# Performance work log

Measured on AMD Instinct MI355X. Metric: run time of the kernel, lower is better.

## Reference

```python
import jax, jax.numpy as jnp
import numpy as np

N_HEAD = 12


def build_mask(T, N):
    """Boolean mask, True = blocked. Mirrors st_mask construction for
    text_mask_mode='none', domain_present=None, text_to_motion_attn=False."""
    L = 3 * T + 5 * N
    r = jnp.arange(T)
    causal = r[:, None] >= r[None, :]          # allowed (lower-tri incl diag)
    strict = r[:, None] > r[None, :]           # allowed (strictly lower)
    m = jnp.zeros((L, L), dtype=bool)
    ml = 3 * T
    # motion-motion region starts fully blocked, then 7 sub-blocks opened
    m = m.at[:ml, :ml].set(True)
    m = m.at[0:T, 0:T].set(~causal)
    m = m.at[T:2 * T, 0:T].set(~causal)
    m = m.at[T:2 * T, T:2 * T].set(~strict)
    m = m.at[T:2 * T, 2 * T:3 * T].set(~strict)
    m = m.at[2 * T:3 * T, 0:T].set(~causal)
    m = m.at[2 * T:3 * T, T:2 * T].set(~causal)
    m = m.at[2 * T:3 * T, 2 * T:3 * T].set(~strict)
    # motion queries -> text keys: blocked by default
    m = m.at[:ml, ml:].set(True)
    # text queries -> motion keys: blocked (text_to_motion_attn=False)
    m = m.at[ml:, :ml].set(True)
    # text_mask_mode='none': up/down motion rows attend ALL text domains
    m = m.at[T:3 * T, ml:].set(False)
    return m


def setup_inputs() -> dict:
    key = jax.random.key(0)
    ks = jax.random.split(key, 9)
    C = 768
    B, T, N = 4, 512, 16
    L = 3 * T + 5 * N
    s = 1.0 / np.sqrt(C)
    return {
        "x": jax.random.normal(ks[0], (B, L, C), dtype=jnp.float32),
        "Wq": jax.random.normal(ks[1], (C, C), dtype=jnp.float32) * s,
        "bq": jax.random.normal(ks[2], (C,), dtype=jnp.float32) * 0.02,
        "Wk": jax.random.normal(ks[3], (C, C), dtype=jnp.float32) * s,
        "bk": jax.random.normal(ks[4], (C,), dtype=jnp.float32) * 0.02,
        "Wv": jax.random.normal(ks[5], (C, C), dtype=jnp.float32) * s,
        "bv": jax.random.normal(ks[6], (C,), dtype=jnp.float32) * 0.02,
        "Wp": jax.random.normal(ks[7], (C, C), dtype=jnp.float32) * s,
        "bp": jax.random.normal(ks[8], (C,), dtype=jnp.float32) * 0.02,
        "T_motion": 512,
        "N": 16,
    }


def reference(x, Wq, bq, Wk, bk, Wv, bv, Wp, bp, T_motion, N):
    B, L, C = x.shape
    nh = N_HEAD
    hd = C // nh
    # projections (torch Linear: x @ W.T + b)
    q = (x @ Wq.T + bq).reshape(B, L, nh, hd).transpose(0, 2, 1, 3)
    k = (x @ Wk.T + bk).reshape(B, L, nh, hd).transpose(0, 2, 1, 3)
    v = (x @ Wv.T + bv).reshape(B, L, nh, hd).transpose(0, 2, 1, 3)
    att = jnp.einsum('bhqd,bhkd->bhqk', q, k) * (1.0 / np.sqrt(hd))
    mask = build_mask(T_motion, N)                 # [L, L], True = blocked
    att = jnp.where(mask[None, None], -jnp.inf, att)
    att = jax.nn.softmax(att, axis=-1)
    y = jnp.einsum('bhqk,bhkd->bhqd', att, v)      # [B, nh, L, hd]
    y = y.transpose(0, 2, 1, 3).reshape(B, L, C)
    return y @ Wp.T + bp
```

## Files before the change

### kernel.cpp

```cpp
#include <hip/hip_runtime.h>

typedef _Float16 half8_t __attribute__((ext_vector_type(8)));
typedef _Float16 half4_t __attribute__((ext_vector_type(4)));
typedef int      int2_t  __attribute__((ext_vector_type(2)));
typedef float    f32x4   __attribute__((ext_vector_type(4)));

#define L_TOT 1616
#define L_PAD 1664
#define ML    1536
#define TT    512
#define CDIM  768
#define HD    64
#define NH    12
#define MTOT  6464

#define QK_SCALE 0.1803368801f
#define FIXED_M 10.0f

#if __has_builtin(__builtin_amdgcn_exp2f)
#define EXP2F(x) __builtin_amdgcn_exp2f(x)
#else
#define EXP2F(x) __expf((x) * 0.69314718056f)
#endif

typedef __attribute__((address_space(3))) void  as3_void;
typedef const __attribute__((address_space(1))) void as1_void;
__device__ __forceinline__ void gload_lds16(const void* g, void* l) {
  __builtin_amdgcn_global_load_lds((as1_void*)g, (as3_void*)l, 16, 0, 0);
}

__device__ __forceinline__ bool is_blocked(int i, int j) {
  if (j >= L_TOT) return true;
  if (i >= ML) return j < ML;
  if (j >= ML) return i < TT;
  int bi = i >> 9, bj = j >> 9;
  int a = i & 511, c = j & 511;
  if (bi == 0) return !(bj == 0 && c <= a);
  if (bi == 1) {
    if (bj == 0) return !(c <= a);
    return !(c < a);
  }
  if (bj == 2) return !(c < a);
  return !(c <= a);
}

__device__ __forceinline__ void mask_interval(int qrow, int k0, int& lo, int& hi) {
  lo = 0; hi = L_TOT - 1;
  if (qrow >= L_TOT)      { hi = -1; }
  else if (qrow >= ML)    { lo = ML; }
  else if (k0 >= ML)      { }
  else {
    int bi = qrow >> 9, bj = k0 >> 9, a = qrow & 511;
    if (bi == 0 && bj > 0) hi = -1;
    else {
      int strict = (bj > 0 && !(bi == 2 && bj == 1)) ? 1 : 0;
      hi = bj * 512 + a - strict;
    }
  }
}

__global__ __launch_bounds__(256) void cvt_kernel(
    const float* __restrict__ x, const float* __restrict__ wq,
    const float* __restrict__ wk, const float* __restrict__ wv,
    const float* __restrict__ wp, _Float16* __restrict__ Xh,
    _Float16* __restrict__ Wh)
{
  const int XN = MTOT * CDIM, WN = CDIM * CDIM;
  int i = (blockIdx.x * 256 + threadIdx.x) * 4;
  const float* src; _Float16* dst;
  if (i < XN) { src = x + i; dst = Xh + i; }
  else {
    int off = i - XN;
    int which = off / WN, rem = off - which * WN;
    const float* w = (which == 0) ? wq : (which == 1) ? wk : (which == 2) ? wv : wp;
    src = w + rem; dst = Wh + off;
  }
  float4 f = *(const float4*)src;
  half4_t h;
  h[0] = (_Float16)f.x; h[1] = (_Float16)f.y;
  h[2] = (_Float16)f.z; h[3] = (_Float16)f.w;
  *(half4_t*)dst = h;
}

__global__ __launch_bounds__(256) void gemm128_kernel(
    const _Float16* __restrict__ A, const _Float16* __restrict__ W,
    const float* __restrict__ bq, const float* __restrict__ bk,
    const float* __restrict__ bv, const float* __restrict__ bp,
    _Float16* __restrict__ Qh, _Float16* __restrict__ Kh,
    _Float16* __restrict__ Vt, float* __restrict__ Out, int fused)
{
  __shared__ __align__(16) _Float16 As[128 * 64];
  __shared__ __align__(16) _Float16 Bs[128 * 64];
  int tm = blockIdx.x, tn = blockIdx.y;
  int tid = threadIdx.x;
  int w = tid >> 6, lane = tid & 63;
  int wm = w & 1, wn = w >> 1;
  int lr = lane & 15, quad = lane >> 4;
  f32x4 acc[4][4];
#pragma unroll
  for (int i = 0; i < 4; i++)
#pragma unroll
    for (int j = 0; j < 4; j++) acc[i][j] = (f32x4){0.f, 0.f, 0.f, 0.f};
  int glog = ((lane & 7) ^ (lane >> 3)) * 8;
  const _Float16* gA[4]; const _Float16* gB[4];
#pragma unroll
  for (int u = 0; u < 4; u++) {
    int rl = (w * 4 + u) * 8 + (lane >> 3);
    int ar = tm * 128 + rl; if (ar >= MTOT) ar = MTOT - 1;
    gA[u] = A + (size_t)ar * CDIM + glog;
    gB[u] = W + (size_t)(tn * 128 + rl) * CDIM + glog;
  }
  const int lsw = lr & 7;
  for (int k0 = 0; k0 < CDIM; k0 += 64) {
    __syncthreads();
#pragma unroll
    for (int u = 0; u < 4; u++) {
      gload_lds16(gA[u] + k0, As + (w * 4 + u) * 512);
      gload_lds16(gB[u] + k0, Bs + (w * 4 + u) * 512);
    }
    __syncthreads();
#pragma unroll
    for (int kg = 0; kg < 8; kg += 4) {
      half8_t a[4], b[4];
#pragma unroll
      for (int g = 0; g < 4; g++) {
        a[g] = *(const half8_t*)(As + (wm * 64 + g * 16 + lr) * 64 + (((quad + kg) ^ lsw) * 8));
        b[g] = *(const half8_t*)(Bs + (wn * 64 + g * 16 + lr) * 64 + (((quad + kg) ^ lsw) * 8));
      }
#pragma unroll
      for (int mg = 0; mg < 4; mg++)
#pragma unroll
        for (int ng = 0; ng < 4; ng++)
          acc[mg][ng] = __builtin_amdgcn_mfma_f32_16x16x32_f16(a[mg], b[ng],
                                                               acc[mg][ng], 0, 0, 0);
    }
  }
  int mat, cbase;
  const float* bias;
  if (fused) { mat = tn / 6; cbase = (tn % 6) * 128;
               bias = (mat == 0) ? bq : (mat == 1) ? bk : bv; }
  else       { mat = 3; cbase = tn * 128; bias = bp; }
#pragma unroll
  for (int mg = 0; mg < 4; mg++) {
#pragma unroll
    for (int ng = 0; ng < 4; ng++) {
      int colt = wn * 64 + ng * 16 + lr;
      int c = cbase + colt;
      float bval = bias[c];
      int h = c >> 6, d = c & 63;
      int m0 = tm * 128 + wm * 64 + mg * 16 + quad * 4;
      if (mat == 3) {
        for (int r = 0; r < 4; r++) {
          int m = m0 + r;
          if (m < MTOT) Out[(size_t)m * CDIM + c] = acc[mg][ng][r] + bval;
        }
      } else if (mat == 2) {
        if (m0 < MTOT) {
          int b = m0 / L_TOT, l0 = m0 - b * L_TOT;
          int l0p = (l0 & ~63) | ((((l0 >> 2) & 3) << 4) | (((l0 >> 4) & 3) << 2));
          half4_t hv;
          for (int r = 0; r < 4; r++) hv[r] = (_Float16)(acc[mg][ng][r] + bval);
          *(half4_t*)&Vt[((size_t)(b * NH + h) * HD + d) * L_PAD + l0p] = hv;
        }
      } else {
        _Float16* dst = (mat == 0) ? Qh : Kh;
        for (int r = 0; r < 4; r++) {
          int m = m0 + r;
          if (m < MTOT) {
            int b = m / L_TOT, l = m - b * L_TOT;
            dst[((size_t)(b * NH + h) * L_PAD + l) * HD + d] = (_Float16)(acc[mg][ng][r] + bval);
          }
        }
      }
    }
  }
}

__global__ __launch_bounds__(256) void attn_kernel(
    const _Float16* __restrict__ Qh, const _Float16* __restrict__ Kh,
    const _Float16* __restrict__ Vt, _Float16* __restrict__ Yh)
{
  __shared__ __align__(16) _Float16 Ks[64 * 64];
  __shared__ __align__(16) _Float16 Vs[64 * 64];
  __shared__ __align__(16) _Float16 Os[64 * 72];
  int qx = blockIdx.x;
  int qt = (qx < 24) ? (23 - qx) : qx;
  int bh = blockIdx.y;
  int b = bh / NH, h = bh - b * NH;
  const _Float16* Qb = Qh + (size_t)bh * L_PAD * HD;
  const _Float16* Kb = Kh + (size_t)bh * L_PAD * HD;
  const _Float16* Vb = Vt + (size_t)bh * HD * L_PAD;
  int tid = threadIdx.x;
  int w = tid >> 6, lane = tid & 63;
  int lr = lane & 15, quad = lane >> 4;
  const int lsw = lr & 7;

  int qrow = qt * 64 + w * 16 + lr;
  half8_t qf0 = *(const half8_t*)(Qb + (size_t)qrow * HD + quad * 8);
  half8_t qf1 = *(const half8_t*)(Qb + (size_t)qrow * HD + 32 + quad * 8);
  {
    _Float16 sc = (_Float16)QK_SCALE;
#pragma unroll
    for (int j = 0; j < 8; j++) { qf0[j] *= sc; qf1[j] *= sc; }
  }

  float l_run = 0.f;
  f32x4 oacc[4];
  for (int mt = 0; mt < 4; mt++) oacc[mt] = (f32x4){0.f, 0.f, 0.f, 0.f};

  int glog = ((lane & 7) ^ (lane >> 3)) * 8;
  const _Float16* pK[2]; const _Float16* pV[2];
  _Float16* ldsK[2]; _Float16* ldsV[2];
#pragma unroll
  for (int u = 0; u < 2; u++) {
    int rl = (w * 2 + u) * 8 + (lane >> 3);
    pK[u] = Kb + (size_t)rl * HD + glog;
    pV[u] = Vb + (size_t)rl * L_PAD + glog;
    ldsK[u] = Ks + (w * 2 + u) * 512;
    ldsV[u] = Vs + (w * 2 + u) * 512;
  }
  const _Float16* kA0 = Ks + lr * 64 + (quad ^ lsw) * 8;
  const _Float16* kA1 = Ks + lr * 64 + (((quad + 4) & 7) ^ lsw) * 8;
  const _Float16* vA0 = Vs + lr * 64 + ((2 * quad) ^ lsw) * 8;
  const _Float16* vA1 = Vs + lr * 64 + ((2 * quad + 1) ^ lsw) * 8;

  int i_max = qt * 64 + 63; if (i_max >= L_TOT) i_max = L_TOT - 1;
  int i_min = qt * 64;

  for (int kt = 0; kt < 26; kt++) {
    int k0 = kt * 64;
    if (is_blocked(i_max, k0)) continue;
    bool full = (kt != 25) && !is_blocked(i_min, k0 + 63);
    __syncthreads();
#pragma unroll
    for (int u = 0; u < 2; u++) {
      gload_lds16(pK[u] + (k0 << 6), ldsK[u]);
      gload_lds16(pV[u] + k0, ldsV[u]);
    }
    __syncthreads();
    f32x4 s4[4];
#pragma unroll
    for (int cg = 0; cg < 4; cg++) {
      half8_t kf0 = *(const half8_t*)(kA0 + cg * 1024);
      half8_t kf1 = *(const half8_t*)(kA1 + cg * 1024);
      f32x4 z = (f32x4){0.f, 0.f, 0.f, 0.f};
      z = __builtin_amdgcn_mfma_f32_16x16x32_f16(kf0, qf0, z, 0, 0, 0);
      z = __builtin_amdgcn_mfma_f32_16x16x32_f16(kf1, qf1, z, 0, 0, 0);
      s4[cg] = z;
    }
    if (!full) {
      int lo, hi;
      mask_interval(qrow, k0, lo, hi);
#pragma unroll
      for (int cg = 0; cg < 4; cg++) {
        int kb = k0 + cg * 16 + quad * 4;
#pragma unroll
        for (int r = 0; r < 4; r++) {
          int j = kb + r;
          if (j < lo || j > hi) s4[cg][r] = -1e30f;
        }
      }
    }
    int packed[8];
    float ladd = 0.f;
#pragma unroll
    for (int cg = 0; cg < 4; cg++) {
      float p0 = EXP2F(s4[cg][0] - FIXED_M);
      float p1 = EXP2F(s4[cg][1] - FIXED_M);
      float p2 = EXP2F(s4[cg][2] - FIXED_M);
      float p3 = EXP2F(s4[cg][3] - FIXED_M);
      ladd += (p0 + p1) + (p2 + p3);
      packed[cg * 2]     = __builtin_bit_cast(int, __builtin_amdgcn_cvt_pkrtz(p0, p1));
      packed[cg * 2 + 1] = __builtin_bit_cast(int, __builtin_amdgcn_cvt_pkrtz(p2, p3));
    }
    l_run += ladd;
#pragma unroll
    for (int p = 0; p < 2; p++) {
      const _Float16* vb = p ? vA1 : vA0;
      int2_t piL; piL[0] = packed[(2 * p) * 2];     piL[1] = packed[(2 * p) * 2 + 1];
      int2_t piH; piH[0] = packed[(2 * p + 1) * 2]; piH[1] = packed[(2 * p + 1) * 2 + 1];
      half4_t pbL = __builtin_bit_cast(half4_t, piL);
      half4_t pbH = __builtin_bit_cast(half4_t, piH);
#pragma unroll
      for (int mt2 = 0; mt2 < 4; mt2++) {
        half8_t v8 = *(const half8_t*)(vb + mt2 * 1024);
        half4_t vlo = __builtin_shufflevector(v8, v8, 0, 1, 2, 3);
        half4_t vhi = __builtin_shufflevector(v8, v8, 4, 5, 6, 7);
        oacc[mt2] = __builtin_amdgcn_mfma_f32_16x16x16f16(vlo, pbL, oacc[mt2], 0, 0, 0);
        oacc[mt2] = __builtin_amdgcn_mfma_f32_16x16x16f16(vhi, pbH, oacc[mt2], 0, 0, 0);
      }
    }
  }
  l_run += __shfl_xor(l_run, 16);
  l_run += __shfl_xor(l_run, 32);
  __syncthreads();
  float inv = 1.f / l_run;
#pragma unroll
  for (int mt2 = 0; mt2 < 4; mt2++)
    for (int r = 0; r < 4; r++)
      Os[(w * 16 + lr) * 72 + mt2 * 16 + quad * 4 + r] =
          (_Float16)(oacc[mt2][r] * inv);
  __syncthreads();
  {
    int rr = w * 16 + (lane >> 2);
    int cc = (lane & 3) * 16;
    int i = qt * 64 + rr;
    if (i < L_TOT) {
      const _Float16* srcp = Os + rr * 72 + cc;
      int4 y0 = *(const int4*)srcp;
      int4 y1 = *(const int4*)(srcp + 8);
      _Float16* dst = Yh + ((size_t)(b * L_TOT) + i) * CDIM + h * HD + cc;
      *(int4*)dst = y0;
      *(int4*)(dst + 8) = y1;
    }
  }
}

extern "C" void kernel_launch(void* const* d_in, const int* in_sizes, int n_in,
                              void* d_out, int out_size, void* d_ws, size_t ws_size,
                              hipStream_t stream)
{
  const float* x  = (const float*)d_in[0];
  const float* Wq = (const float*)d_in[1];
  const float* bq = (const float*)d_in[2];
  const float* Wk = (const float*)d_in[3];
  const float* bk = (const float*)d_in[4];
  const float* Wv = (const float*)d_in[5];
  const float* bv = (const float*)d_in[6];
  const float* Wp = (const float*)d_in[7];
  const float* bp = (const float*)d_in[8];
  float* out = (float*)d_out;

  _Float16* ws = (_Float16*)d_ws;
  const size_t XN  = (size_t)MTOT * CDIM;
  const size_t WN  = (size_t)CDIM * CDIM;
  const size_t XNP = (size_t)48 * L_PAD * HD;
  _Float16* Xh = ws;
  _Float16* Wh = Xh + XN;
  _Float16* Qh = Wh + 4 * WN;
  _Float16* Kh = Qh + XNP;
  _Float16* Vt = Kh + XNP;
  _Float16* Yh = Xh;

  const int cvt_blocks = (int)((XN + 4 * WN) / 4 / 256);
  cvt_kernel<<<cvt_blocks, 256, 0, stream>>>(x, Wq, Wk, Wv, Wp, Xh, Wh);
  gemm128_kernel<<<dim3(51, 18), 256, 0, stream>>>(Xh, Wh, bq, bk, bv, bp,
                                                   Qh, Kh, Vt, out, 1);
  attn_kernel<<<dim3(26, 48), 256, 0, stream>>>(Qh, Kh, Vt, Yh);
  gemm128_kernel<<<dim3(51, 6), 256, 0, stream>>>(Yh, Wh + 3 * WN, bq, bk, bv, bp,
                                                  Qh, Kh, Vt, out, 0);
}
```

Baseline: 213.8 us.

## Double-buffer K/V tiles in attention and swizzle GEMM block order for L2 reuse

The attention kernel now keeps two LDS buffers for the K and V tiles. It issues the async global-to-LDS loads for the next unmasked tile before computing on the current one, with vmcnt waits and raw barriers in place of the two syncthreads per iteration. This is meant to hide global load latency behind the MFMA work. Separately, the GEMM launches become a 1D grid remapped into 8-row-band supertiles, for better L2 reuse of A and W; the padded blocks past the last row tile exit early. The larger LDS footprint (32KB) may lower occupancy.

```diff
diff --git a/kernel.cpp b/kernel.cpp
--- a/kernel.cpp
+++ b/kernel.cpp
@@ -91,7 +91,13 @@
 {
   __shared__ __align__(16) _Float16 As[128 * 64];
   __shared__ __align__(16) _Float16 Bs[128 * 64];
-  int tm = blockIdx.x, tn = blockIdx.y;
+  int stcols = fused ? 3 : 1;
+  int id = blockIdx.x;
+  int st = id / 48, local = id - st * 48;
+  int band = st / stcols, stc = st - band * stcols;
+  int tm = band * 8 + (local & 7);
+  int tn = stc * 6 + (local >> 3);
+  if (tm >= 51) return;
   int tid = threadIdx.x;
   int w = tid >> 6, lane = tid & 63;
   int wm = w & 1, wn = w >> 1;
@@ -180,9 +186,7 @@
     const _Float16* __restrict__ Qh, const _Float16* __restrict__ Kh,
     const _Float16* __restrict__ Vt, _Float16* __restrict__ Yh)
 {
-  __shared__ __align__(16) _Float16 Ks[64 * 64];
-  __shared__ __align__(16) _Float16 Vs[64 * 64];
-  __shared__ __align__(16) _Float16 Os[64 * 72];
+  __shared__ __align__(16) _Float16 smem[16384];
   int qx = blockIdx.x;
   int qt = (qx < 24) ? (23 - qx) : qx;
   int bh = blockIdx.y;
@@ -210,90 +214,112 @@
 
   int glog = ((lane & 7) ^ (lane >> 3)) * 8;
   const _Float16* pK[2]; const _Float16* pV[2];
-  _Float16* ldsK[2]; _Float16* ldsV[2];
 #pragma unroll
   for (int u = 0; u < 2; u++) {
     int rl = (w * 2 + u) * 8 + (lane >> 3);
     pK[u] = Kb + (size_t)rl * HD + glog;
     pV[u] = Vb + (size_t)rl * L_PAD + glog;
-    ldsK[u] = Ks + (w * 2 + u) * 512;
-    ldsV[u] = Vs + (w * 2 + u) * 512;
-  }
-  const _Float16* kA0 = Ks + lr * 64 + (quad ^ lsw) * 8;
-  const _Float16* kA1 = Ks + lr * 64 + (((quad + 4) & 7) ^ lsw) * 8;
-  const _Float16* vA0 = Vs + lr * 64 + ((2 * quad) ^ lsw) * 8;
-  const _Float16* vA1 = Vs + lr * 64 + ((2 * quad + 1) ^ lsw) * 8;
+  }
+  int dmaOff0 = (w * 2) * 512, dmaOff1 = (w * 2 + 1) * 512;
+  const int kOff0 = lr * 64 + (quad ^ lsw) * 8;
+  const int kOff1 = lr * 64 + (((quad + 4) & 7) ^ lsw) * 8;
+  const int vOff0 = lr * 64 + ((2 * quad) ^ lsw) * 8;
+  const int vOff1 = lr * 64 + ((2 * quad + 1) ^ lsw) * 8;
 
   int i_max = qt * 64 + 63; if (i_max >= L_TOT) i_max = L_TOT - 1;
   int i_min = qt * 64;
 
-  for (int kt = 0; kt < 26; kt++) {
+  auto issue = [&](int kt, int buf) {
     int k0 = kt * 64;
-    if (is_blocked(i_max, k0)) continue;
-    bool full = (kt != 25) && !is_blocked(i_min, k0 + 63);
-    __syncthreads();
-#pragma unroll
-    for (int u = 0; u < 2; u++) {
-      gload_lds16(pK[u] + (k0 << 6), ldsK[u]);
-      gload_lds16(pV[u] + k0, ldsV[u]);
-    }
-    __syncthreads();
-    f32x4 s4[4];
-#pragma unroll
-    for (int cg = 0; cg < 4; cg++) {
-      half8_t kf0 = *(const half8_t*)(kA0 + cg * 1024);
-      half8_t kf1 = *(const half8_t*)(kA1 + cg * 1024);
-      f32x4 z = (f32x4){0.f, 0.f, 0.f, 0.f};
-      z = __builtin_amdgcn_mfma_f32_16x16x32_f16(kf0, qf0, z, 0, 0, 0);
-      z = __builtin_amdgcn_mfma_f32_16x16x32_f16(kf1, qf1, z, 0, 0, 0);
-      s4[cg] = z;
-    }
-    if (!full) {
-      int lo, hi;
-      mask_interval(qrow, k0, lo, hi);
+    _Float16* kb = smem + buf * 4096;
+    _Float16* vb = smem + 8192 + buf * 4096;
+    gload_lds16(pK[0] + ((size_t)k0 << 6), kb + dmaOff0);
+    gload_lds16(pK[1] + ((size_t)k0 << 6), kb + dmaOff1);
+    gload_lds16(pV[0] + k0, vb + dmaOff0);
+    gload_lds16(pV[1] + k0, vb + dmaOff1);
+  };
+
+  int kt_cur = 0;
+  while (is_blocked(i_max, kt_cur * 64)) kt_cur++;
+  int cur = 0;
+  issue(kt_cur, 0);
+  for (;;) {
+    int kn = kt_cur + 1;
+    while (kn < 26 && is_blocked(i_max, kn * 64)) kn++;
+    bool has_next = (kn < 26);
+    if (has_next) {
+      issue(kn, cur ^ 1);
+      asm volatile("s_waitcnt vmcnt(4)" ::: "memory");
+    } else {
+      asm volatile("s_waitcnt vmcnt(0)" ::: "memory");
+    }
+    asm volatile("s_barrier" ::: "memory");
+    {
+      int k0 = kt_cur * 64;
+      bool full = (kt_cur != 25) && !is_blocked(i_min, k0 + 63);
+      const _Float16* kb = smem + cur * 4096;
+      const _Float16* vb = smem + 8192 + cur * 4096;
+      f32x4 s4[4];
 #pragma unroll
       for (int cg = 0; cg < 4; cg++) {
-        int kb = k0 + cg * 16 + quad * 4;
-#pragma unroll
-        for (int r = 0; r < 4; r++) {
-          int j = kb + r;
-          if (j < lo || j > hi) s4[cg][r] = -1e30f;
-        }
-      }
-    }
-    int packed[8];
-    float ladd = 0.f;
-#pragma unroll
-    for (int cg = 0; cg < 4; cg++) {
-      float p0 = EXP2F(s4[cg][0] - FIXED_M);
-      float p1 = EXP2F(s4[cg][1] - FIXED_M);
-      float p2 = EXP2F(s4[cg][2] - FIXED_M);
-      float p3 = EXP2F(s4[cg][3] - FIXED_M);
-      ladd += (p0 + p1) + (p2 + p3);
-      packed[cg * 2]     = __builtin_bit_cast(int, __builtin_amdgcn_cvt_pkrtz(p0, p1));
-      packed[cg * 2 + 1] = __builtin_bit_cast(int, __builtin_amdgcn_cvt_pkrtz(p2, p3));
-    }
-    l_run += ladd;
-#pragma unroll
-    for (int p = 0; p < 2; p++) {
-      const _Float16* vb = p ? vA1 : vA0;
-      int2_t piL; piL[0] = packed[(2 * p) * 2];     piL[1] = packed[(2 * p) * 2 + 1];
-      int2_t piH; piH[0] = packed[(2 * p + 1) * 2]; piH[1] = packed[(2 * p + 1) * 2 + 1];
-      half4_t pbL = __builtin_bit_cast(half4_t, piL);
-      half4_t pbH = __builtin_bit_cast(half4_t, piH);
-#pragma unroll
-      for (int mt2 = 0; mt2 < 4; mt2++) {
-        half8_t v8 = *(const half8_t*)(vb + mt2 * 1024);
-        half4_t vlo = __builtin_shufflevector(v8, v8, 0, 1, 2, 3);
-        half4_t vhi = __builtin_shufflevector(v8, v8, 4, 5, 6, 7);
-        oacc[mt2] = __builtin_amdgcn_mfma_f32_16x16x16f16(vlo, pbL, oacc[mt2], 0, 0, 0);
-        oacc[mt2] = __builtin_amdgcn_mfma_f32_16x16x16f16(vhi, pbH, oacc[mt2], 0, 0, 0);
-      }
-    }
+        half8_t kf0 = *(const half8_t*)(kb + kOff0 + cg * 1024);
+        half8_t kf1 = *(const half8_t*)(kb + kOff1 + cg * 1024);
+        f32x4 z = (f32x4){0.f, 0.f, 0.f, 0.f};
+        z = __builtin_amdgcn_mfma_f32_16x16x32_f16(kf0, qf0, z, 0, 0, 0);
+        z = __builtin_amdgcn_mfma_f32_16x16x32_f16(kf1, qf1, z, 0, 0, 0);
+        s4[cg] = z;
+      }
+      if (!full) {
+        int lo, hi;
+        mask_interval(qrow, k0, lo, hi);
+#pragma unroll
+        for (int cg = 0; cg < 4; cg++) {
+          int kbs = k0 + cg * 16 + quad * 4;
+#pragma unroll
+          for (int r = 0; r < 4; r++) {
+            int j = kbs + r;
+            if (j < lo || j > hi) s4[cg][r] = -1e30f;
+          }
+        }
+      }
+      int packed[8];
+      float ladd = 0.f;
+#pragma unroll
+      for (int cg = 0; cg < 4; cg++) {
+        float p0 = EXP2F(s4[cg][0] - FIXED_M);
+        float p1 = EXP2F(s4[cg][1] - FIXED_M);
+        float p2 = EXP2F(s4[cg][2] - FIXED_M);
+        float p3 = EXP2F(s4[cg][3] - FIXED_M);
+        ladd += (p0 + p1) + (p2 + p3);
+        packed[cg * 2]     = __builtin_bit_cast(int, __builtin_amdgcn_cvt_pkrtz(p0, p1));
+        packed[cg * 2 + 1] = __builtin_bit_cast(int, __builtin_amdgcn_cvt_pkrtz(p2, p3));
+      }
+      l_run += ladd;
+#pragma unroll
+      for (int p = 0; p < 2; p++) {
+        const _Float16* vbp = vb + (p ? vOff1 : vOff0);
+        int2_t piL; piL[0] = packed[(2 * p) * 2];     piL[1] = packed[(2 * p) * 2 + 1];
+        int2_t piH; piH[0] = packed[(2 * p + 1) * 2]; piH[1] = packed[(2 * p + 1) * 2 + 1];
+        half4_t pbL = __builtin_bit_cast(half4_t, piL);
+        half4_t pbH = __builtin_bit_cast(half4_t, piH);
+#pragma unroll
+        for (int mt2 = 0; mt2 < 4; mt2++) {
+          half8_t v8 = *(const half8_t*)(vbp + mt2 * 1024);
+          half4_t vlo = __builtin_shufflevector(v8, v8, 0, 1, 2, 3);
+          half4_t vhi = __builtin_shufflevector(v8, v8, 4, 5, 6, 7);
+          oacc[mt2] = __builtin_amdgcn_mfma_f32_16x16x16f16(vlo, pbL, oacc[mt2], 0, 0, 0);
+          oacc[mt2] = __builtin_amdgcn_mfma_f32_16x16x16f16(vhi, pbH, oacc[mt2], 0, 0, 0);
+        }
+      }
+    }
+    if (!has_next) break;
+    asm volatile("s_barrier" ::: "memory");
+    kt_cur = kn; cur ^= 1;
   }
   l_run += __shfl_xor(l_run, 16);
   l_run += __shfl_xor(l_run, 32);
   __syncthreads();
+  _Float16* Os = smem;
   float inv = 1.f / l_run;
 #pragma unroll
   for (int mt2 = 0; mt2 < 4; mt2++)
@@ -344,9 +370,9 @@
 
   const int cvt_blocks = (int)((XN + 4 * WN) / 4 / 256);
   cvt_kernel<<<cvt_blocks, 256, 0, stream>>>(x, Wq, Wk, Wv, Wp, Xh, Wh);
-  gemm128_kernel<<<dim3(51, 18), 256, 0, stream>>>(Xh, Wh, bq, bk, bv, bp,
-                                                   Qh, Kh, Vt, out, 1);
+  gemm128_kernel<<<dim3(1008), 256, 0, stream>>>(Xh, Wh, bq, bk, bv, bp,
+                                                 Qh, Kh, Vt, out, 1);
   attn_kernel<<<dim3(26, 48), 256, 0, stream>>>(Qh, Kh, Vt, Yh);
-  gemm128_kernel<<<dim3(51, 6), 256, 0, stream>>>(Yh, Wh + 3 * WN, bq, bk, bv, bp,
-                                                  Qh, Kh, Vt, out, 0);
-}
+  gemm128_kernel<<<dim3(336), 256, 0, stream>>>(Yh, Wh + 3 * WN, bq, bk, bv, bp,
+                                                Qh, Kh, Vt, out, 0);
+}
```

Result: faster. 206.0 us (-3.6%).

## Swizzle GEMM/attention block order for L2 reuse and load K/V directly to registers

Applied to the files above, without the earlier changes.

The GEMM grid becomes a 1D launch remapped into 8-row-tile by 6-column-tile supertiles, so neighbouring blocks share A and W tiles in cache. The attention grid is made bh-fastest so the 48 heads of one q-tile are scheduled together. Attention also drops the LDS staging of K/V tiles and its two barriers per iteration, and instead has each wave load its MFMA fragments straight from global memory. This removes the synchronisation, but each wave now reads K/V itself, raising global/L2 traffic and leaving less latency hiding.

```diff
diff --git a/kernel.cpp b/kernel.cpp
--- a/kernel.cpp
+++ b/kernel.cpp
@@ -91,7 +91,13 @@
 {
   __shared__ __align__(16) _Float16 As[128 * 64];
   __shared__ __align__(16) _Float16 Bs[128 * 64];
-  int tm = blockIdx.x, tn = blockIdx.y;
+  int stcols = fused ? 3 : 1;
+  int id = blockIdx.x;
+  int st = id / 48, local = id - st * 48;
+  int band = st / stcols, stc = st - band * stcols;
+  int tm = band * 8 + (local & 7);
+  int tn = stc * 6 + (local >> 3);
+  if (tm >= 51) return;
   int tid = threadIdx.x;
   int w = tid >> 6, lane = tid & 63;
   int wm = w & 1, wn = w >> 1;
@@ -180,12 +186,10 @@
     const _Float16* __restrict__ Qh, const _Float16* __restrict__ Kh,
     const _Float16* __restrict__ Vt, _Float16* __restrict__ Yh)
 {
-  __shared__ __align__(16) _Float16 Ks[64 * 64];
-  __shared__ __align__(16) _Float16 Vs[64 * 64];
   __shared__ __align__(16) _Float16 Os[64 * 72];
-  int qx = blockIdx.x;
+  int id = blockIdx.x;
+  int qx = id / 48, bh = id - qx * 48;
   int qt = (qx < 24) ? (23 - qx) : qx;
-  int bh = blockIdx.y;
   int b = bh / NH, h = bh - b * NH;
   const _Float16* Qb = Qh + (size_t)bh * L_PAD * HD;
   const _Float16* Kb = Kh + (size_t)bh * L_PAD * HD;
@@ -193,7 +197,6 @@
   int tid = threadIdx.x;
   int w = tid >> 6, lane = tid & 63;
   int lr = lane & 15, quad = lane >> 4;
-  const int lsw = lr & 7;
 
   int qrow = qt * 64 + w * 16 + lr;
   half8_t qf0 = *(const half8_t*)(Qb + (size_t)qrow * HD + quad * 8);
@@ -208,21 +211,8 @@
   f32x4 oacc[4];
   for (int mt = 0; mt < 4; mt++) oacc[mt] = (f32x4){0.f, 0.f, 0.f, 0.f};
 
-  int glog = ((lane & 7) ^ (lane >> 3)) * 8;
-  const _Float16* pK[2]; const _Float16* pV[2];
-  _Float16* ldsK[2]; _Float16* ldsV[2];
-#pragma unroll
-  for (int u = 0; u < 2; u++) {
-    int rl = (w * 2 + u) * 8 + (lane >> 3);
-    pK[u] = Kb + (size_t)rl * HD + glog;
-    pV[u] = Vb + (size_t)rl * L_PAD + glog;
-    ldsK[u] = Ks + (w * 2 + u) * 512;
-    ldsV[u] = Vs + (w * 2 + u) * 512;
-  }
-  const _Float16* kA0 = Ks + lr * 64 + (quad ^ lsw) * 8;
-  const _Float16* kA1 = Ks + lr * 64 + (((quad + 4) & 7) ^ lsw) * 8;
-  const _Float16* vA0 = Vs + lr * 64 + ((2 * quad) ^ lsw) * 8;
-  const _Float16* vA1 = Vs + lr * 64 + ((2 * quad + 1) ^ lsw) * 8;
+  const _Float16* kBase = Kb + (size_t)lr * HD + quad * 8;
+  const _Float16* vBase = Vb + (size_t)lr * L_PAD + quad * 16;
 
   int i_max = qt * 64 + 63; if (i_max >= L_TOT) i_max = L_TOT - 1;
   int i_min = qt * 64;
@@ -231,21 +221,25 @@
     int k0 = kt * 64;
     if (is_blocked(i_max, k0)) continue;
     bool full = (kt != 25) && !is_blocked(i_min, k0 + 63);
-    __syncthreads();
-#pragma unroll
-    for (int u = 0; u < 2; u++) {
-      gload_lds16(pK[u] + (k0 << 6), ldsK[u]);
-      gload_lds16(pV[u] + k0, ldsV[u]);
-    }
-    __syncthreads();
+    half8_t kf0[4], kf1[4];
+#pragma unroll
+    for (int cg = 0; cg < 4; cg++) {
+      const _Float16* kp = kBase + (size_t)(k0 + cg * 16) * HD;
+      kf0[cg] = *(const half8_t*)kp;
+      kf1[cg] = *(const half8_t*)(kp + 32);
+    }
+    half8_t vf[2][4];
+#pragma unroll
+    for (int p = 0; p < 2; p++)
+#pragma unroll
+      for (int mt2 = 0; mt2 < 4; mt2++)
+        vf[p][mt2] = *(const half8_t*)(vBase + (size_t)(mt2 * 16) * L_PAD + k0 + p * 8);
     f32x4 s4[4];
 #pragma unroll
     for (int cg = 0; cg < 4; cg++) {
-      half8_t kf0 = *(const half8_t*)(kA0 + cg * 1024);
-      half8_t kf1 = *(const half8_t*)(kA1 + cg * 1024);
       f32x4 z = (f32x4){0.f, 0.f, 0.f, 0.f};
-      z = __builtin_amdgcn_mfma_f32_16x16x32_f16(kf0, qf0, z, 0, 0, 0);
-      z = __builtin_amdgcn_mfma_f32_16x16x32_f16(kf1, qf1, z, 0, 0, 0);
+      z = __builtin_amdgcn_mfma_f32_16x16x32_f16(kf0[cg], qf0, z, 0, 0, 0);
+      z = __builtin_amdgcn_mfma_f32_16x16x32_f16(kf1[cg], qf1, z, 0, 0, 0);
       s4[cg] = z;
     }
     if (!full) {
@@ -253,10 +247,10 @@
       mask_interval(qrow, k0, lo, hi);
 #pragma unroll
       for (int cg = 0; cg < 4; cg++) {
-        int kb = k0 + cg * 16 + quad * 4;
+        int kbs = k0 + cg * 16 + quad * 4;
 #pragma unroll
         for (int r = 0; r < 4; r++) {
-          int j = kb + r;
+          int j = kbs + r;
           if (j < lo || j > hi) s4[cg][r] = -1e30f;
         }
       }
@@ -276,14 +270,13 @@
     l_run += ladd;
 #pragma unroll
     for (int p = 0; p < 2; p++) {
-      const _Float16* vb = p ? vA1 : vA0;
       int2_t piL; piL[0] = packed[(2 * p) * 2];     piL[1] = packed[(2 * p) * 2 + 1];
       int2_t piH; piH[0] = packed[(2 * p + 1) * 2]; piH[1] = packed[(2 * p + 1) * 2 + 1];
       half4_t pbL = __builtin_bit_cast(half4_t, piL);
       half4_t pbH = __builtin_bit_cast(half4_t, piH);
 #pragma unroll
       for (int mt2 = 0; mt2 < 4; mt2++) {
-        half8_t v8 = *(const half8_t*)(vb + mt2 * 1024);
+        half8_t v8 = vf[p][mt2];
         half4_t vlo = __builtin_shufflevector(v8, v8, 0, 1, 2, 3);
         half4_t vhi = __builtin_shufflevector(v8, v8, 4, 5, 6, 7);
         oacc[mt2] = __builtin_amdgcn_mfma_f32_16x16x16f16(vlo, pbL, oacc[mt2], 0, 0, 0);
@@ -293,7 +286,6 @@
   }
   l_run += __shfl_xor(l_run, 16);
   l_run += __shfl_xor(l_run, 32);
-  __syncthreads();
   float inv = 1.f / l_run;
 #pragma unroll
   for (int mt2 = 0; mt2 < 4; mt2++)
@@ -344,9 +336,9 @@
 
   const int cvt_blocks = (int)((XN + 4 * WN) / 4 / 256);
   cvt_kernel<<<cvt_blocks, 256, 0, stream>>>(x, Wq, Wk, Wv, Wp, Xh, Wh);
-  gemm128_kernel<<<dim3(51, 18), 256, 0, stream>>>(Xh, Wh, bq, bk, bv, bp,
-                                                   Qh, Kh, Vt, out, 1);
-  attn_kernel<<<dim3(26, 48), 256, 0, stream>>>(Qh, Kh, Vt, Yh);
-  gemm128_kernel<<<dim3(51, 6), 256, 0, stream>>>(Yh, Wh + 3 * WN, bq, bk, bv, bp,
-                                                  Qh, Kh, Vt, out, 0);
-}
+  gemm128_kernel<<<dim3(1008), 256, 0, stream>>>(Xh, Wh, bq, bk, bv, bp,
+                                                 Qh, Kh, Vt, out, 1);
+  attn_kernel<<<dim3(26 * 48), 256, 0, stream>>>(Qh, Kh, Vt, Yh);
+  gemm128_kernel<<<dim3(336), 256, 0, stream>>>(Yh, Wh + 3 * WN, bq, bk, bv, bp,
+                                                Qh, Kh, Vt, out, 0);
+}
```

After: 279.4 us. +30.7%, slower.
